# Kernel tuning notes

Measured on AMD Instinct MI355X. Metric: run time of the kernel, lower is better.

## Reference

```python
import jax, jax.numpy as jnp
import numpy as np

PATCH = 9          # patch_size
DILATION_PATCH = 1 # dilation_patch


def _bilinear_sample(img, px, py):
    """Bilinear sample img [b,c,H,W] at pixel coords px,py [b,P,h,w].
    Matches torch grid_sample(mode='bilinear', align_corners=True,
    padding_mode='zeros'): each out-of-bounds corner contributes zero.
    Returns [b,P,h,w,c]."""
    b, c, H, W = img.shape
    flat = img.transpose(0, 2, 3, 1).reshape(b, H * W, c)  # [b,HW,c]
    x0 = jnp.floor(px)
    y0 = jnp.floor(py)
    wx1 = px - x0
    wx0 = 1.0 - wx1
    wy1 = py - y0
    wy0 = 1.0 - wy1
    x0i = x0.astype(jnp.int32)
    y0i = y0.astype(jnp.int32)
    x1i = x0i + 1
    y1i = y0i + 1

    def gather(ix, iy):
        valid = ((ix >= 0) & (ix <= W - 1) & (iy >= 0) & (iy <= H - 1))
        idx = jnp.clip(iy, 0, H - 1) * W + jnp.clip(ix, 0, W - 1)  # [b,P,h,w]
        g = jnp.take_along_axis(flat, idx.reshape(b, -1, 1), axis=1)
        g = g.reshape(*ix.shape, c)
        return g * valid[..., None].astype(img.dtype)

    return ((wy0 * wx0)[..., None] * gather(x0i, y0i)
            + (wy0 * wx1)[..., None] * gather(x1i, y0i)
            + (wy1 * wx0)[..., None] * gather(x0i, y1i)
            + (wy1 * wx1)[..., None] * gather(x1i, y1i))


def setup_inputs() -> dict:
    key = jax.random.key(0)
    k1, k2, k3 = jax.random.split(key, 3)
    b, c, h, w = 2, 128, 64, 96
    return {
        "input1": jax.random.normal(k1, (b, c, h, w), dtype=jnp.float32),
        "input2": jax.random.normal(k2, (b, c, h, w), dtype=jnp.float32),
        "flow": jax.random.normal(k3, (b, 2, h, w), dtype=jnp.float32),
    }


def reference(input1, input2, flow):
    # kernel_size=1, stride=1, padding=0, dilation=1 (defaults supported by module)
    b, c, H, W = input2.shape
    dt = input1.dtype
    # absolute coordinate grid (x = horizontal, y = vertical), then translate by flow
    gy, gx = jnp.meshgrid(jnp.arange(H, dtype=dt), jnp.arange(W, dtype=dt), indexing='ij')
    cx = gx[None] + flow[:, 0]  # [b,h,w]
    cy = gy[None] + flow[:, 1]
    # patch offsets in pixels. The torch code normalizes to [-1,1] and samples with
    # align_corners=True, which is exactly equivalent to these pixel-space coords.
    off = DILATION_PATCH * ((PATCH - 1) // 2)
    offs = jnp.arange(PATCH, dtype=dt) * DILATION_PATCH - off
    dy, dx = jnp.meshgrid(offs, offs, indexing='ij')
    dy = dy.reshape(-1)  # [P]
    dx = dx.reshape(-1)
    px = cx[:, None] + dx[None, :, None, None]  # [b,P,h,w]
    py = cy[:, None] + dy[None, :, None, None]
    sampled = _bilinear_sample(input2, px, py)            # [b,P,h,w,c]
    corr = jnp.einsum('bphwc,bchw->bphw', sampled, input1)
    return corr.reshape(b, PATCH, PATCH, H, W)
```

## Files before the change

kernel.cpp:

```cpp
#include <hip/hip_runtime.h>

#define HH  64
#define WW  96
#define CC  128
#define BB  2
#define HWI (HH*WW)

#define PXB  8
#define TCOL 28
#define ROWB (TCOL*64)
#define BUFB (20*ROWB)
#define NCHK 35
#define AOFF BUFB
#define ASTR 272
#define LDSZ (AOFF + 16*ASTR)

typedef __attribute__((ext_vector_type(8))) _Float16 half8;
typedef __attribute__((ext_vector_type(4))) _Float16 half4;
typedef __attribute__((ext_vector_type(4))) float    f32x4;
typedef unsigned int u32;

__device__ __forceinline__ void gll16(const void* g, void* l) {
    __builtin_amdgcn_global_load_lds(
        (const __attribute__((address_space(1))) u32*)g,
        (__attribute__((address_space(3))) u32*)l, 16, 0, 0);
}

__global__ __launch_bounds__(256) void conv_i2(const float* __restrict__ I2,
                                               unsigned char* __restrict__ I2t)
{
    const int bid  = blockIdx.x;
    const int tid  = threadIdx.x;
    const int xcd  = bid & 7;
    const int s    = bid >> 3;
    const int b    = xcd >> 2;
    const int band = xcd & 3;
    const int kc   = s / 6;
    const int cs   = s - kc*6;
    const int g    = tid & 3;
    const int cq   = cs*4 + ((tid >> 2) & 3);
    const int row  = band*16 + (tid >> 4);
    const int col0 = cq*4;

    const float* src = I2 + ((size_t)(b*CC + kc*32 + g*8)*HH + row)*WW + col0;
    float va[8][4];
#pragma unroll
    for (int j = 0; j < 8; ++j) {
        const float4 v = *(const float4*)(src + (size_t)j*HWI);
        va[j][0] = v.x; va[j][1] = v.y; va[j][2] = v.z; va[j][3] = v.w;
    }

    unsigned char* dst = I2t + (size_t)(((b*4 + kc)*HH + row)*WW + col0)*64;
    const int sbase = g ^ (cq & 3);
#pragma unroll
    for (int k = 0; k < 4; ++k) {
        half8 h;
#pragma unroll
        for (int j = 0; j < 8; ++j) h[j] = (_Float16)va[j][k];
        *(half8*)(dst + k*64 + ((sbase ^ k) << 4)) = h;
    }
}

__global__ __launch_bounds__(256, 4) void corr_kernel(
    const float* __restrict__ I1,
    const unsigned char* __restrict__ I2t,
    const float* __restrict__ flow,
    float* __restrict__ out)
{
    __shared__ __align__(16) unsigned char smem[LDSZ];

    const int tid  = threadIdx.x;
    const int lane = tid & 63;
    const int w    = tid >> 6;

    const int bid = blockIdx.x;
    const int xcd = bid & 7;
    const int j   = bid >> 3;
    const int b   = xcd >> 2;
    const int y0  = 16*(xcd & 3) + 2*(j & 7);
    const int X   = (j >> 3) * PXB;

    const int s_tile = min(max(X - 9, 0), WW - TCOL);

    const int fpx = lane & 15;
    const int kg  = lane >> 4;

    const int cpx = tid & 7;
    const int oq  = tid >> 3;
    const int xx  = X + cpx;
    float cxv[2], cyv[2];
#pragma unroll
    for (int yloc = 0; yloc < 2; ++yloc) {
        const int yy = y0 + yloc;
        cxv[yloc] = (float)xx + flow[((size_t)(b*2+0)*HH + yy)*WW + xx];
        cyv[yloc] = (float)yy + flow[((size_t)(b*2+1)*HH + yy)*WW + xx];
    }

#pragma unroll
    for (int i = 0; i < 2; ++i) {
        const int e   = tid + 256*i;
        const int q   = e & 1;
        const int ch  = (e >> 1) & 127;
        const int myy = e >> 8;
        const float4 v = *(const float4*)&I1[((size_t)(b*CC + ch)*HH + y0 + myy)*WW + X + q*4];
        const float ve[4] = { v.x, v.y, v.z, v.w };
#pragma unroll
        for (int k = 0; k < 4; ++k) {
            const int m = myy*8 + q*4 + k;
            *(_Float16*)(smem + AOFF + m*ASTR + ch*2) = (_Float16)ve[k];
        }
    }

    int boff[9];
#pragma unroll
    for (int i = 0; i < 9; ++i) {
        const int t   = min(w + 4*i, NCHK - 1);
        const int n   = t*16 + fpx;
        const int r_t = n / TCOL;
        const int c_t = n - r_t*TCOL;
        const int col = s_tile + c_t;
        boff[i] = r_t*ROWB + c_t*64 + ((kg ^ ((col ^ (col >> 2)) & 3)) << 4);
    }
    const int aoff = AOFF + fpx*ASTR + (kg << 4);

    auto stage = [&](int rr) {
#pragma unroll
        for (int i = 0; i < 9; ++i) {
            const int p = w + 4*i;
            if (p < NCHK) {
                const int z   = p*1024 + lane*16;
                const int r_t = z / ROWB;
                const int off = z - r_t*ROWB;
                const int c   = off >> 6;
                const int lb  = off & 63;
                const int grow = min(max(y0 - 9 + r_t, 0), HH - 1);
                const unsigned char* src = I2t
                    + ((size_t)(((b*4 + rr)*HH + grow)*WW + s_tile + c))*64 + lb;
                gll16(src, smem + p*1024);
            }
        }
    };

    f32x4 acc[9];
#pragma unroll
    for (int i = 0; i < 9; ++i) acc[i] = (f32x4){0.f,0.f,0.f,0.f};

    stage(0);
    __syncthreads();

#pragma unroll
    for (int r = 0; r < 4; ++r) {
        const half8 af = *(const half8*)(smem + aoff + r*64);
#pragma unroll
        for (int i = 0; i < 9; ++i) {
            if (w + 4*i < NCHK) {
                const half8 bf = *(const half8*)(smem + boff[i]);
                acc[i] = __builtin_amdgcn_mfma_f32_16x16x32_f16(af, bf, acc[i], 0, 0, 0);
            }
        }
        __syncthreads();
        if (r < 3) {
            stage(r + 1);
            __syncthreads();
        }
    }

    _Float16* D = (_Float16*)smem;
#pragma unroll
    for (int i = 0; i < 9; ++i) {
        if (w + 4*i < NCHK) {
            const int n   = (w + 4*i)*16 + fpx;
            const int r_t = n / TCOL;
            const int c_t = n - r_t*TCOL;
            const half4 hv = { (_Float16)acc[i][0], (_Float16)acc[i][1],
                               (_Float16)acc[i][2], (_Float16)acc[i][3] };
            *(half4*)(D + (c_t*21 + r_t)*20 + kg*4) = hv;
        }
    }
    __syncthreads();

#pragma unroll
    for (int yloc = 0; yloc < 2; ++yloc) {
        const int yy = y0 + yloc;
        const int m  = yloc*8 + cpx;
        const float cx = cxv[yloc], cy = cyv[yloc];
        const int x0c = (int)floorf(cx);
        const int y0c = (int)floorf(cy);
        const float wx1 = cx - (float)x0c, wx0 = 1.f - wx1;
        const float wy1 = cy - (float)y0c, wy0 = 1.f - wy1;
        float* outb = out + (size_t)b*81*HWI + (size_t)yy*WW + xx;

#pragma unroll
        for (int k = 0; k < 3; ++k) {
            const int o = oq + 32*k;
            if (o < 81) {
                const int dyi = o / 9;
                const int dxi = o - dyi*9;
                const int ix0 = x0c - 4 + dxi;
                const int iy0 = y0c - 4 + dyi;
                const bool vx0 = (ix0   >= 0) && (ix0   < WW);
                const bool vx1 = (ix0+1 >= 0) && (ix0+1 < WW);
                const bool vy0 = (iy0   >= 0) && (iy0   < HH);
                const bool vy1 = (iy0+1 >= 0) && (iy0+1 < HH);
                const int rt  = iy0 - y0 + 9;
                const int r0c = min(max(rt,     0), 19);
                const int r1c = min(max(rt + 1, 0), 19);
                const int c0  = ix0 - s_tile;
                const int c0c = min(max(c0,     0), TCOL-1);
                const int c1c = min(max(c0 + 1, 0), TCOL-1);
                const float d00 = (float)D[(c0c*21 + r0c)*20 + m];
                const float d01 = (float)D[(c1c*21 + r0c)*20 + m];
                const float d10 = (float)D[(c0c*21 + r1c)*20 + m];
                const float d11 = (float)D[(c1c*21 + r1c)*20 + m];
                const float r0 = (vx0 ? wx0*d00 : 0.f) + (vx1 ? wx1*d01 : 0.f);
                const float r1 = (vx0 ? wx0*d10 : 0.f) + (vx1 ? wx1*d11 : 0.f);
                const float v  = (vy0 ? wy0*r0 : 0.f) + (vy1 ? wy1*r1 : 0.f);
                outb[(size_t)o*HWI] = v;
            }
        }
    }
}

extern "C" void kernel_launch(void* const* d_in, const int* in_sizes, int n_in,
                              void* d_out, int out_size, void* d_ws, size_t ws_size,
                              hipStream_t stream)
{
    const float* I1   = (const float*)d_in[0];
    const float* I2   = (const float*)d_in[1];
    const float* flow = (const float*)d_in[2];
    float* out = (float*)d_out;
    unsigned char* I2t = (unsigned char*)d_ws;

    conv_i2<<<dim3(192), dim3(256), 0, stream>>>(I2, I2t);
    corr_kernel<<<dim3(768), dim3(256), 0, stream>>>(I1, I2t, flow, out);
}
```

Before: 20.08 us.

## Widen correlation tile to 16 pixels per block with 512 threads

Result: no change. 20.22 us (+0.7%).

```diff
diff --git a/kernel.cpp b/kernel.cpp
--- a/kernel.cpp
+++ b/kernel.cpp
@@ -6,14 +6,15 @@
 #define BB  2
 #define HWI (HH*WW)
 
-#define PXB  8
-#define TCOL 28
+#define PXB  16
+#define TCOL 36
 #define ROWB (TCOL*64)
 #define BUFB (20*ROWB)
-#define NCHK 35
+#define NCHK 45
 #define AOFF BUFB
 #define ASTR 272
-#define LDSZ (AOFF + 16*ASTR)
+#define LDSZ (AOFF + 32*ASTR)
+#define DM   36
 
 typedef __attribute__((ext_vector_type(8))) _Float16 half8;
 typedef __attribute__((ext_vector_type(4))) _Float16 half4;
@@ -61,7 +62,7 @@
     }
 }
 
-__global__ __launch_bounds__(256, 4) void corr_kernel(
+__global__ __launch_bounds__(512, 4) void corr_kernel(
     const float* __restrict__ I1,
     const unsigned char* __restrict__ I2t,
     const float* __restrict__ flow,
@@ -80,13 +81,15 @@
     const int y0  = 16*(xcd & 3) + 2*(j & 7);
     const int X   = (j >> 3) * PXB;
 
-    const int s_tile = min(max(X - 9, 0), WW - TCOL);
+    const int s_tile = min(max(X - 10, 0), WW - TCOL);
 
     const int fpx = lane & 15;
     const int kg  = lane >> 4;
-
-    const int cpx = tid & 7;
-    const int oq  = tid >> 3;
+    const int my  = w & 1;
+    const int nw  = w >> 1;
+
+    const int cpx = tid & 15;
+    const int oq  = (tid >> 4) & 31;
     const int xx  = X + cpx;
     float cxv[2], cyv[2];
 #pragma unroll
@@ -98,35 +101,35 @@
 
 #pragma unroll
     for (int i = 0; i < 2; ++i) {
-        const int e   = tid + 256*i;
-        const int q   = e & 1;
-        const int ch  = (e >> 1) & 127;
-        const int myy = e >> 8;
-        const float4 v = *(const float4*)&I1[((size_t)(b*CC + ch)*HH + y0 + myy)*WW + X + q*4];
+        const int e    = tid + 512*i;
+        const int q    = e & 3;
+        const int ch   = (e >> 2) & 127;
+        const int yloc = e >> 9;
+        const float4 v = *(const float4*)&I1[((size_t)(b*CC + ch)*HH + y0 + yloc)*WW + X + q*4];
         const float ve[4] = { v.x, v.y, v.z, v.w };
 #pragma unroll
         for (int k = 0; k < 4; ++k) {
-            const int m = myy*8 + q*4 + k;
+            const int m = yloc*16 + q*4 + k;
             *(_Float16*)(smem + AOFF + m*ASTR + ch*2) = (_Float16)ve[k];
         }
     }
 
-    int boff[9];
-#pragma unroll
-    for (int i = 0; i < 9; ++i) {
-        const int t   = min(w + 4*i, NCHK - 1);
+    int boff[12];
+#pragma unroll
+    for (int i = 0; i < 12; ++i) {
+        const int t   = min(nw + 4*i, NCHK - 1);
         const int n   = t*16 + fpx;
         const int r_t = n / TCOL;
         const int c_t = n - r_t*TCOL;
         const int col = s_tile + c_t;
         boff[i] = r_t*ROWB + c_t*64 + ((kg ^ ((col ^ (col >> 2)) & 3)) << 4);
     }
-    const int aoff = AOFF + fpx*ASTR + (kg << 4);
+    const int aoff = AOFF + (my*16 + fpx)*ASTR + (kg << 4);
 
     auto stage = [&](int rr) {
 #pragma unroll
-        for (int i = 0; i < 9; ++i) {
-            const int p = w + 4*i;
+        for (int i = 0; i < 6; ++i) {
+            const int p = w + 8*i;
             if (p < NCHK) {
                 const int z   = p*1024 + lane*16;
                 const int r_t = z / ROWB;
@@ -141,9 +144,9 @@
         }
     };
 
-    f32x4 acc[9];
-#pragma unroll
-    for (int i = 0; i < 9; ++i) acc[i] = (f32x4){0.f,0.f,0.f,0.f};
+    f32x4 acc[12];
+#pragma unroll
+    for (int i = 0; i < 12; ++i) acc[i] = (f32x4){0.f,0.f,0.f,0.f};
 
     stage(0);
     __syncthreads();
@@ -152,8 +155,8 @@
     for (int r = 0; r < 4; ++r) {
         const half8 af = *(const half8*)(smem + aoff + r*64);
 #pragma unroll
-        for (int i = 0; i < 9; ++i) {
-            if (w + 4*i < NCHK) {
+        for (int i = 0; i < 12; ++i) {
+            if (nw + 4*i < NCHK) {
                 const half8 bf = *(const half8*)(smem + boff[i]);
                 acc[i] = __builtin_amdgcn_mfma_f32_16x16x32_f16(af, bf, acc[i], 0, 0, 0);
             }
@@ -167,14 +170,14 @@
 
     _Float16* D = (_Float16*)smem;
 #pragma unroll
-    for (int i = 0; i < 9; ++i) {
-        if (w + 4*i < NCHK) {
-            const int n   = (w + 4*i)*16 + fpx;
+    for (int i = 0; i < 12; ++i) {
+        if (nw + 4*i < NCHK) {
+            const int n   = (nw + 4*i)*16 + fpx;
             const int r_t = n / TCOL;
             const int c_t = n - r_t*TCOL;
             const half4 hv = { (_Float16)acc[i][0], (_Float16)acc[i][1],
                                (_Float16)acc[i][2], (_Float16)acc[i][3] };
-            *(half4*)(D + (c_t*21 + r_t)*20 + kg*4) = hv;
+            *(half4*)(D + (c_t*21 + r_t)*DM + my*16 + kg*4) = hv;
         }
     }
     __syncthreads();
@@ -182,7 +185,7 @@
 #pragma unroll
     for (int yloc = 0; yloc < 2; ++yloc) {
         const int yy = y0 + yloc;
-        const int m  = yloc*8 + cpx;
+        const int m  = yloc*16 + cpx;
         const float cx = cxv[yloc], cy = cyv[yloc];
         const int x0c = (int)floorf(cx);
         const int y0c = (int)floorf(cy);
@@ -208,10 +211,10 @@
                 const int c0  = ix0 - s_tile;
                 const int c0c = min(max(c0,     0), TCOL-1);
                 const int c1c = min(max(c0 + 1, 0), TCOL-1);
-                const float d00 = (float)D[(c0c*21 + r0c)*20 + m];
-                const float d01 = (float)D[(c1c*21 + r0c)*20 + m];
-                const float d10 = (float)D[(c0c*21 + r1c)*20 + m];
-                const float d11 = (float)D[(c1c*21 + r1c)*20 + m];
+                const float d00 = (float)D[(c0c*21 + r0c)*DM + m];
+                const float d01 = (float)D[(c1c*21 + r0c)*DM + m];
+                const float d10 = (float)D[(c0c*21 + r1c)*DM + m];
+                const float d11 = (float)D[(c1c*21 + r1c)*DM + m];
                 const float r0 = (vx0 ? wx0*d00 : 0.f) + (vx1 ? wx1*d01 : 0.f);
                 const float r1 = (vx0 ? wx0*d10 : 0.f) + (vx1 ? wx1*d11 : 0.f);
                 const float v  = (vy0 ? wy0*r0 : 0.f) + (vy1 ? wy1*r1 : 0.f);
@@ -232,5 +235,5 @@
     unsigned char* I2t = (unsigned char*)d_ws;
 
     conv_i2<<<dim3(192), dim3(256), 0, stream>>>(I2, I2t);
-    corr_kernel<<<dim3(768), dim3(256), 0, stream>>>(I1, I2t, flow, out);
-}
+    corr_kernel<<<dim3(384), dim3(512), 0, stream>>>(I1, I2t, flow, out);
+}
```
